# Kernel optimization log

Measured on AMD Instinct MI355X. Metric: run time of the kernel, lower is better.

## Reference

```python
import jax, jax.numpy as jnp
import numpy as np

M, L, P, KK = 8, 3, 12, 9  # n_heads, n_levels, n_points, patch_size**2

def lrelu(v):
    return jnp.where(v >= 0, v, 0.1 * v)

def conv2d(x, w, b, pad):
    y = jax.lax.conv_general_dilated(x, w, (1, 1), [(pad, pad), (pad, pad)], dimension_numbers=('NCHW', 'OIHW', 'NCHW'))
    return y + b[None, :, None, None]

def trunk(x, w1, b1, w2, b2, w3, b3, w4, b4):
    h = lrelu(conv2d(x, w1, b1, 0))
    h = lrelu(conv2d(h, w2, b2, 1))
    h = lrelu(conv2d(h, w3, b3, 1))
    return conv2d(h, w4, b4, 0)

def grid_sample(img, gx, gy, align_corners):
    # img [N,C,H,W]; gx,gy [N,Q] normalized to [-1,1]; bilinear, zeros padding
    N, C, H, W = img.shape
    if align_corners:
        ix = (gx + 1.0) * 0.5 * (W - 1)
        iy = (gy + 1.0) * 0.5 * (H - 1)
    else:
        ix = ((gx + 1.0) * W - 1.0) * 0.5
        iy = ((gy + 1.0) * H - 1.0) * 0.5
    ix0 = jnp.floor(ix); iy0 = jnp.floor(iy)
    wx1 = ix - ix0; wy1 = iy - iy0
    flat = img.reshape(N, C, H * W)
    def gather(xi, yi, wgt):
        valid = (xi >= 0) & (xi <= W - 1) & (yi >= 0) & (yi <= H - 1)
        idx = (jnp.clip(yi, 0, H - 1) * W + jnp.clip(xi, 0, W - 1)).astype(jnp.int32)
        v = jnp.take_along_axis(flat, idx[:, None, :], axis=2)
        return v * (wgt * valid)[:, None, :]
    return (gather(ix0, iy0, (1 - wx1) * (1 - wy1)) + gather(ix0 + 1, iy0, wx1 * (1 - wy1))
            + gather(ix0, iy0 + 1, (1 - wx1) * wy1) + gather(ix0 + 1, iy0 + 1, wx1 * wy1))

def flow_warp(img, flow):
    # img [n,c,h,w]; flow [n,2,h,w] in pixels; torch grid_sample align_corners=True, zeros padding
    n, c, h, w = img.shape
    gy, gx = jnp.meshgrid(jnp.arange(h, dtype=img.dtype), jnp.arange(w, dtype=img.dtype), indexing='ij')
    gxn = 2.0 * (gx[None] + flow[:, 0]) / max(w - 1, 1) - 1.0
    gyn = 2.0 * (gy[None] + flow[:, 1]) / max(h - 1, 1) - 1.0
    return grid_sample(img, gxn.reshape(n, -1), gyn.reshape(n, -1), True).reshape(n, c, h, w)

def msdeform_attn(value, loc, attn, h, w):
    # pytorch MSDeformAttn core: value [N,L*HW,M,D]; loc [N,HW,M,L,Pt,2]; attn [N,HW,M,L,Pt]
    N, _, _, D = value.shape
    HW = h * w
    Pt = loc.shape[4]
    grids = 2.0 * loc - 1.0
    sampled = []
    for l in range(L):
        v = value[:, l * HW:(l + 1) * HW].transpose(0, 2, 3, 1).reshape(N * M, D, h, w)
        g = grids[:, :, :, l].transpose(0, 2, 1, 3, 4).reshape(N * M, HW * Pt, 2)
        s = grid_sample(v, g[..., 0], g[..., 1], False)  # [N*M, D, HW*Pt]
        sampled.append(s.reshape(N * M, D, HW, Pt))
    sampled = jnp.concatenate(sampled, axis=-1)  # [N*M, D, HW, L*Pt]
    aw = attn.transpose(0, 2, 1, 3, 4).reshape(N * M, HW, L * Pt)
    out = jnp.einsum('ndqp,nqp->nqd', sampled, aw)
    return out.reshape(N, M, HW, D).transpose(0, 2, 1, 3).reshape(N, HW, M * D)

def _forward(x, flow_1, flow_2, flip_flow_1, flip_flow_2, aw_w1, aw_b1, aw_w2, aw_b2, aw_w3, aw_b3, aw_w4, aw_b4, so_w1, so_b1, so_w2, so_b2, so_w3, so_b3, so_w4, so_b4, po_w1, po_b1, po_w2, po_b2, po_w3, po_b3, po_w4, po_b4, vp_w, vp_b, op_w1, op_b1, op_w2, op_b2):
    n, t, c, h, w = x.shape
    HW = h * w
    flow_cn1 = flow_1
    flow_cn2 = flow_1 + flow_warp(flow_2, flow_cn1)
    warp1 = flow_warp(x[:, 1], flow_cn1)
    warp2 = flow_warp(x[:, 2], flow_cn2)
    extra = jnp.concatenate([x[:, 0], warp1, warp2, flow_cn1, flow_cn2], axis=1)  # [n, 3c+4, h, w]
    value = conv2d(x.reshape(n, t * c, h, w), vp_w, vp_b, 0)
    off = trunk(extra, so_w1, so_b1, so_w2, so_b2, so_w3, so_b3, so_w4, so_b4)
    aw = trunk(extra, aw_w1, aw_b1, aw_w2, aw_b2, aw_w3, aw_b3, aw_w4, aw_b4)
    po = trunk(extra, po_w1, po_b1, po_w2, po_b2, po_w3, po_b3, po_w4, po_b4)
    value = value.reshape(n, t, c, HW).transpose(0, 1, 3, 2).reshape(n, t * HW, M, c // M)
    off = off.reshape(n, -1, HW).transpose(0, 2, 1).reshape(n, HW, M, L, P, 2)
    po = po.reshape(n, -1, HW).transpose(0, 2, 1).reshape(n, HW, M, L, P)
    po = jax.nn.sigmoid(po) * 3.0
    aw = aw.reshape(n, -1, HW).transpose(0, 2, 1).reshape(n, HW, M, L * P * KK)
    aw = jax.nn.softmax(aw, axis=-1).reshape(n, HW, M, L, P * KK)
    # flow-guided per-level offsets: level0 zeros, level1 flow_cn1, level2 flow_cn2
    f1 = flow_cn1.reshape(n, 2, HW).transpose(0, 2, 1)
    f2 = flow_cn2.reshape(n, 2, HW).transpose(0, 2, 1)
    fstack = jnp.stack([jnp.zeros_like(f1), f1, f2], axis=2)  # [n,HW,L,2]
    off = off + fstack[:, :, None, :, None, :]
    # 3x3 patch around each sampling point, scaled by learned patch offsets
    a = jnp.arange(-1, 2, dtype=x.dtype)
    pnx, pny = jnp.meshgrid(a, a, indexing='ij')
    p_n = jnp.stack([pnx, pny], axis=-1).reshape(KK, 2)
    off = off[..., None, :] + p_n * po[..., None, None]  # [n,HW,M,L,P,KK,2]
    off = off.reshape(n, HW, M, L, P * KK, 2)
    # reference points (valid ratios == 1)
    ry = (jnp.arange(h, dtype=x.dtype) + 0.5) / h
    rx = (jnp.arange(w, dtype=x.dtype) + 0.5) / w
    gy, gx = jnp.meshgrid(ry, rx, indexing='ij')
    ref = jnp.stack([gx, gy], axis=-1).reshape(1, HW, 1, 1, 1, 2)
    norm = jnp.array([w, h], dtype=x.dtype)
    loc = ref + off / norm
    out = msdeform_attn(value, loc, aw, h, w)  # [n, HW, c]
    feat = out.reshape(n, h, w, c).transpose(0, 3, 1, 2)
    res = conv2d(lrelu(conv2d(feat, op_w1, op_b1, 0)), op_w2, op_b2, 0)
    return res + x[:, 0]

def setup_inputs():
    key = jax.random.key(0)
    keys = jax.random.split(key, 64)
    it = iter(range(64))
    def nrm(shape, scale):
        return jax.random.normal(keys[next(it)], shape, jnp.float32) * scale
    n, t, c, h, w = 1, 3, 64, 64, 64
    Cin = t * c + 4  # 196
    d = {}
    d['x'] = nrm((n, t, c, h, w), 1.0)
    for nm in ['flow_1', 'flow_2', 'flip_flow_1', 'flip_flow_2']:
        d[nm] = nrm((n, 2, h, w), 1.5)
    def branch(prefix, out_ch, final_scale):
        d[prefix + '_w1'] = nrm((64, Cin, 1, 1), 1.0 / np.sqrt(Cin))
        d[prefix + '_b1'] = nrm((64,), 0.01)
        d[prefix + '_w2'] = nrm((64, 64, 3, 3), 1.0 / np.sqrt(64 * 9))
        d[prefix + '_b2'] = nrm((64,), 0.01)
        d[prefix + '_w3'] = nrm((64, 64, 3, 3), 1.0 / np.sqrt(64 * 9))
        d[prefix + '_b3'] = nrm((64,), 0.01)
        d[prefix + '_w4'] = nrm((out_ch, 64, 1, 1), final_scale)
        d[prefix + '_b4'] = nrm((out_ch,), 0.01)
    branch('aw', M * L * P * KK, 0.01)
    branch('so', M * L * P * 2, 0.01)
    branch('po', M * L * P, 0.01)
    d['vp_w'] = nrm((t * c, t * c, 1, 1), 1.0 / np.sqrt(t * c))
    d['vp_b'] = nrm((t * c,), 0.01)
    d['op_w1'] = nrm((c, c, 1, 1), 1.0 / np.sqrt(c))
    d['op_b1'] = nrm((c,), 0.01)
    d['op_w2'] = nrm((c, c, 1, 1), 1.0 / np.sqrt(c))
    d['op_b2'] = nrm((c,), 0.01)
    return d

def reference(x, flow_1, flow_2, flip_flow_1, flip_flow_2, aw_w1, aw_b1, aw_w2, aw_b2, aw_w3, aw_b3, aw_w4, aw_b4, so_w1, so_b1, so_w2, so_b2, so_w3, so_b3, so_w4, so_b4, po_w1, po_b1, po_w2, po_b2, po_w3, po_b3, po_w4, po_b4, vp_w, vp_b, op_w1, op_b1, op_w2, op_b2):
    return _forward(x, flow_1, flow_2, flip_flow_1, flip_flow_2, aw_w1, aw_b1, aw_w2, aw_b2, aw_w3, aw_b3, aw_w4, aw_b4, so_w1, so_b1, so_w2, so_b2, so_w3, so_b3, so_w4, so_b4, po_w1, po_b1, po_w2, po_b2, po_w3, po_b3, po_w4, po_b4, vp_w, vp_b, op_w1, op_b1, op_w2, op_b2)
```

## Files before the change

kernel.cpp:

```cpp
#include <hip/hip_runtime.h>
#include <hip/hip_bf16.h>
#include <math.h>

#define HWN 4096
#define VROW 72
#define VYP 36
#define VSZ_SH (24 * VYP * VROW * 16)

typedef __attribute__((ext_vector_type(8))) short short8;
typedef __attribute__((ext_vector_type(4))) float f32x4;

__device__ __forceinline__ float lrelu_f(float v) { return v >= 0.f ? v : 0.1f * v; }

__device__ __forceinline__ unsigned short f2bf(float f) {
  union { float f; unsigned u; } v; v.f = f;
  unsigned r = v.u + 0x7fff + ((v.u >> 16) & 1);
  return (unsigned short)(r >> 16);
}
__device__ __forceinline__ float bf2f(unsigned short u) {
  union { unsigned u; float f; } v; v.u = ((unsigned)u) << 16;
  return v.f;
}
__device__ __forceinline__ float bf_lo(unsigned u) {
  union { unsigned u; float f; } v; v.u = u << 16; return v.f;
}
__device__ __forceinline__ float bf_hi(unsigned u) {
  union { unsigned u; float f; } v; v.u = u & 0xffff0000u; return v.f;
}

__device__ __forceinline__ float bilin_zero(const float* __restrict__ img, float ix, float iy) {
  float fx0 = floorf(ix), fy0 = floorf(iy);
  int x0 = (int)fx0, y0 = (int)fy0;
  float wx1 = ix - fx0, wy1 = iy - fy0;
  float wx0 = 1.f - wx1, wy0 = 1.f - wy1;
  float acc = 0.f;
  if ((unsigned)y0 < 64u) {
    if ((unsigned)x0 < 64u)       acc += wx0 * wy0 * img[y0 * 64 + x0];
    if ((unsigned)(x0 + 1) < 64u) acc += wx1 * wy0 * img[y0 * 64 + x0 + 1];
  }
  if ((unsigned)(y0 + 1) < 64u) {
    if ((unsigned)x0 < 64u)       acc += wx0 * wy1 * img[(y0 + 1) * 64 + x0];
    if ((unsigned)(x0 + 1) < 64u) acc += wx1 * wy1 * img[(y0 + 1) * 64 + x0 + 1];
  }
  return acc;
}

__global__ void k_pre(
    const float* __restrict__ x, const float* __restrict__ flow1, const float* __restrict__ flow2,
    const float* so_w4, const float* po_w4, const float* aw_w4,
    const float* so_b4, const float* po_b4, const float* aw_b4,
    const float* so_b1, const float* po_b1, const float* aw_b1,
    const float* so_b2, const float* po_b2, const float* aw_b2,
    const float* so_b3, const float* po_b3, const float* aw_b3,
    const float* so_w1, const float* po_w1, const float* aw_w1,
    const float* so_w2, const float* po_w2, const float* aw_w2,
    const float* so_w3, const float* po_w3, const float* aw_w3,
    const float* op_w1, const float* op_w2, const float* vp_w,
    unsigned short* Wtail, float* btail, float* b1c, float* b2c, float* b3c,
    unsigned short* o1b, unsigned short* o2b, unsigned short* W1,
    unsigned short* W2g, unsigned short* W3g, unsigned short* vpb,
    unsigned short* xb, float* fcn2, unsigned short* vA) {
  __shared__ unsigned short tile[64 * 65];
  __shared__ unsigned short wrow[576];
  int gx = blockIdx.x;
  int tid = threadIdx.x;
  if (gx < 864) {
    int t = gx * 256 + tid;
    int row = t >> 6, k = t & 63;
    float v = row < 576 ? so_w4[row * 64 + k]
            : row < 864 ? po_w4[(row - 576) * 64 + k]
                        : aw_w4[(row - 864) * 64 + k];
    Wtail[t] = f2bf(v);
  } else if (gx < 912) {
    int t = (gx - 864) * 256 + tid;
    if (t < 3456) {
      btail[t] = t < 576 ? so_b4[t] : t < 864 ? po_b4[t - 576] : aw_b4[t - 864];
    } else if (t < 3648) {
      int i = t - 3456; b1c[i] = i < 64 ? so_b1[i] : i < 128 ? po_b1[i - 64] : aw_b1[i - 128];
    } else if (t < 3840) {
      int i = t - 3648; b2c[i] = i < 64 ? so_b2[i] : i < 128 ? po_b2[i - 64] : aw_b2[i - 128];
    } else if (t < 4032) {
      int i = t - 3840; b3c[i] = i < 64 ? so_b3[i] : i < 128 ? po_b3[i - 64] : aw_b3[i - 128];
    } else if (t < 8128) {
      o1b[t - 4032] = f2bf(op_w1[t - 4032]);
    } else if (t < 12224) {
      o2b[t - 8128] = f2bf(op_w2[t - 8128]);
    }
  } else if (gx < 1080) {
    int t = (gx - 912) * 256 + tid;
    if (t < 192 * 224) {
      int row = t / 224, k = t % 224;
      int tr = row >> 6, lco = row & 63;
      const float* s = tr == 0 ? so_w1 : tr == 1 ? po_w1 : aw_w1;
      W1[t] = (k < 196) ? f2bf(s[lco * 196 + k]) : (unsigned short)0;
    }
  } else if (gx < 1464) {
    int b = gx - 1080;
    int which = b >= 192;
    b &= 191;
    int tr = b >> 6, co = b & 63;
    const float* s;
    if (!which) s = tr == 0 ? so_w2 : tr == 1 ? po_w2 : aw_w2;
    else        s = tr == 0 ? so_w3 : tr == 1 ? po_w3 : aw_w3;
    unsigned short* d = which ? W3g : W2g;
#pragma unroll
    for (int j = tid; j < 576; j += 256) wrow[j] = f2bf(s[co * 576 + j]);
    __syncthreads();
#pragma unroll
    for (int j = tid; j < 576; j += 256)
      d[((size_t)tr * 64 + co) * 576 + j] = wrow[(j & 63) * 9 + (j >> 6)];
  } else if (gx < 1608) {
    int t = (gx - 1464) * 256 + tid;
    if (t < 192 * 192) vpb[t] = f2bf(vp_w[t]);
  } else if (gx < 1800) {
    int b = gx - 1608;
    int ptile = b & 63, cg = b >> 6;
    int px = tid & 63, ch0 = (tid >> 6) * 16;
#pragma unroll
    for (int i = 0; i < 16; i++) {
      float v = x[(size_t)(cg * 64 + ch0 + i) * HWN + ptile * 64 + px];
      tile[(ch0 + i) * 65 + px] = f2bf(v);
    }
    __syncthreads();
    int c = tid & 63, pl0 = (tid >> 6) * 16;
#pragma unroll
    for (int i = 0; i < 16; i++)
      xb[(size_t)(ptile * 64 + pl0 + i) * 192 + cg * 64 + c] = tile[c * 65 + pl0 + i];
  } else if (gx < 1816) {
    int p = (gx - 1800) * 256 + tid;
    int px = p & 63, py = p >> 6;
    float fx = flow1[p], fy = flow1[HWN + p];
    float ix = (float)px + fx, iy = (float)py + fy;
    fcn2[p] = fx + bilin_zero(flow2, ix, iy);
    fcn2[HWN + p] = fy + bilin_zero(flow2 + HWN, ix, iy);
  } else {
    int i = (gx - 1816) * 256 + tid;
    if (i < 2 * VSZ_SH / 8) ((uint4*)vA)[i] = make_uint4(0, 0, 0, 0);
  }
}

__global__ void k_extra(const unsigned short* __restrict__ xb, const float* __restrict__ flow1,
                        const float* __restrict__ fcn2, unsigned short* __restrict__ extra) {
  int w = threadIdx.x >> 6, c = threadIdx.x & 63;
  int p = blockIdx.x * 4 + w;
  int px = p & 63, py = p >> 6;
  float fx1 = flow1[p], fy1 = flow1[HWN + p];
  float fx2 = fcn2[p],  fy2 = fcn2[HWN + p];
  extra[(size_t)p * 224 + c] = xb[(size_t)p * 192 + c];
#pragma unroll
  for (int lev = 0; lev < 2; lev++) {
    float ix = (float)px + (lev ? fx2 : fx1);
    float iy = (float)py + (lev ? fy2 : fy1);
    float fx0 = floorf(ix), fy0 = floorf(iy);
    int x0 = (int)fx0, y0 = (int)fy0;
    float wx1 = ix - fx0, wy1 = iy - fy0;
    float wx0 = 1.f - wx1, wy0 = 1.f - wy1;
    int coff = (lev + 1) * 64;
    float acc = 0.f;
    if ((unsigned)y0 < 64u) {
      if ((unsigned)x0 < 64u)       acc += wx0 * wy0 * bf2f(xb[(size_t)(y0 * 64 + x0) * 192 + coff + c]);
      if ((unsigned)(x0 + 1) < 64u) acc += wx1 * wy0 * bf2f(xb[(size_t)(y0 * 64 + x0 + 1) * 192 + coff + c]);
    }
    if ((unsigned)(y0 + 1) < 64u) {
      if ((unsigned)x0 < 64u)       acc += wx0 * wy1 * bf2f(xb[(size_t)((y0 + 1) * 64 + x0) * 192 + coff + c]);
      if ((unsigned)(x0 + 1) < 64u) acc += wx1 * wy1 * bf2f(xb[(size_t)((y0 + 1) * 64 + x0 + 1) * 192 + coff + c]);
    }
    extra[(size_t)p * 224 + coff + c] = f2bf(acc);
  }
  if (c < 2) {
    extra[(size_t)p * 224 + 192 + c] = f2bf(flow1[c * HWN + p]);
    extra[(size_t)p * 224 + 194 + c] = f2bf(fcn2[c * HWN + p]);
  }
  if (c < 28) extra[(size_t)p * 224 + 196 + c] = 0;
}

__global__ __launch_bounds__(128) void k_gemm2(
    const unsigned short* __restrict__ A0, const unsigned short* __restrict__ Wm0,
    const float* __restrict__ bias0, unsigned short* __restrict__ out0,
    const unsigned short* __restrict__ A1, const unsigned short* __restrict__ Wm1,
    const float* __restrict__ bias1, unsigned short* __restrict__ out1) {
  int z = blockIdx.z;
  const unsigned short* A = z ? A1 : A0;
  const unsigned short* Wm = z ? Wm1 : Wm0;
  const float* bias = z ? bias1 : bias0;
  unsigned short* out = z ? out1 : out0;
  int K = z ? 224 : 192;

  int wv = threadIdx.x >> 6;
  int l = threadIdx.x & 63;
  int lm = l & 15, lq = l >> 4;
  int p0 = blockIdx.x * 32 + wv * 16;
  int co0 = blockIdx.y * 32;

  f32x4 acc[2];
#pragma unroll
  for (int nt = 0; nt < 2; nt++) {
    float bv = bias[co0 + nt * 16 + lm];
    acc[nt] = (f32x4){bv, bv, bv, bv};
  }
  const unsigned short* ap = A + (size_t)(p0 + lm) * K + lq * 8;
  const unsigned short* wp = Wm + (size_t)(co0 + lm) * K + lq * 8;
  for (int k0 = 0; k0 < K; k0 += 32) {
    short8 af = *(const short8*)(ap + k0);
#pragma unroll
    for (int nt = 0; nt < 2; nt++) {
      short8 bf = *(const short8*)(wp + (size_t)nt * 16 * K + k0);
      acc[nt] = __builtin_amdgcn_mfma_f32_16x16x32_bf16(af, bf, acc[nt], 0, 0, 0);
    }
  }
#pragma unroll
  for (int nt = 0; nt < 2; nt++) {
    int co = co0 + nt * 16 + lm;
#pragma unroll
    for (int r = 0; r < 4; r++) {
      int p = p0 + lq * 4 + r;
      float v = acc[nt][r];
      if (z) v = lrelu_f(v);
      out[(size_t)p * 192 + co] = f2bf(v);
    }
  }
}

__global__ __launch_bounds__(128) void k_conv3g(const unsigned short* __restrict__ h,
                                                const unsigned short* __restrict__ Wm,
                                                const float* __restrict__ bias,
                                                unsigned short* __restrict__ out) {
  int wv = threadIdx.x >> 6;
  int l = threadIdx.x & 63;
  int lm = l & 15, lq = l >> 4;
  int p0 = blockIdx.x * 32 + wv * 16;
  int co0 = blockIdx.y * 16;
  int t = blockIdx.z;
  int p = p0 + lm;
  int px = p & 63, py = p >> 6;

  float bv = bias[t * 64 + co0 + lm];
  f32x4 acc = (f32x4){bv, bv, bv, bv};
  const unsigned short* wp = Wm + ((size_t)t * 64 + co0 + lm) * 576 + lq * 8;
#pragma unroll
  for (int kidx = 0; kidx < 9; kidx++) {
    int ky = kidx / 3, kx = kidx % 3;
    int pp = p + (ky - 1) * 64 + (kx - 1);
    bool valid = ((unsigned)(px + kx - 1) < 64u) && ((unsigned)(py + ky - 1) < 64u);
    const unsigned short* apb = h + (size_t)pp * 192 + t * 64 + lq * 8;
#pragma unroll
    for (int c2 = 0; c2 < 2; c2++) {
      short8 af = {};
      if (valid) af = *(const short8*)(apb + c2 * 32);
      short8 bf = *(const short8*)(wp + kidx * 64 + c2 * 32);
      acc = __builtin_amdgcn_mfma_f32_16x16x32_bf16(af, bf, acc, 0, 0, 0);
    }
  }
#pragma unroll
  for (int r = 0; r < 4; r++) {
    int po_ = p0 + lq * 4 + r;
    out[(size_t)po_ * 192 + t * 64 + co0 + lm] = f2bf(lrelu_f(acc[r]));
  }
}

__global__ __launch_bounds__(256) void k_tail(const unsigned short* __restrict__ A,
                                              const unsigned short* __restrict__ Wm,
                                              const float* __restrict__ bias,
                                              unsigned short* __restrict__ out,
                                              const unsigned short* __restrict__ vsb,
                                              unsigned short* __restrict__ vA,
                                              unsigned short* __restrict__ vB) {
  if (blockIdx.y >= 108) {
    int i = ((blockIdx.y - 108) * 64 + blockIdx.x) * 256 + threadIdx.x;
    int lm = i % 24, p = i / 24;
    uint4 v = ((const uint4*)vsb)[p * 24 + lm];
    int y = p >> 6, xx = p & 63;
    int ypA = (y >> 1) + 1, slotA = y & 1;
    int ypB = (y + 1) >> 1, slotB = (y & 1) ^ 1;
    ((uint4*)vA)[((lm * VYP + ypA) * VROW + xx + 2) * 2 + slotA] = v;
    ((uint4*)vB)[((lm * VYP + ypB) * VROW + xx + 2) * 2 + slotB] = v;
    return;
  }
  int wv = threadIdx.x >> 6;
  int l = threadIdx.x & 63;
  int lm = l & 15, lq = l >> 4;
  int p0 = blockIdx.x * 64 + wv * 16;
  int co0 = blockIdx.y * 32;
  int t = (co0 < 576) ? 0 : (co0 < 864 ? 1 : 2);

  f32x4 acc[2];
#pragma unroll
  for (int nt = 0; nt < 2; nt++) {
    float bv = bias[co0 + nt * 16 + lm];
    acc[nt] = (f32x4){bv, bv, bv, bv};
  }
  const unsigned short* ap = A + (size_t)(p0 + lm) * 192 + t * 64 + lq * 8;
  const unsigned short* wp = Wm + (size_t)(co0 + lm) * 64 + lq * 8;
#pragma unroll
  for (int k0 = 0; k0 < 64; k0 += 32) {
    short8 af = *(const short8*)(ap + k0);
#pragma unroll
    for (int nt = 0; nt < 2; nt++) {
      short8 bf = *(const short8*)(wp + (size_t)nt * 16 * 64 + k0);
      acc[nt] = __builtin_amdgcn_mfma_f32_16x16x32_bf16(af, bf, acc[nt], 0, 0, 0);
    }
  }
#pragma unroll
  for (int nt = 0; nt < 2; nt++) {
    int co = co0 + nt * 16 + lm;
#pragma unroll
    for (int r = 0; r < 4; r++) {
      int p = p0 + lq * 4 + r;
      float v = acc[nt][r];
      if (t == 2) v = __expf(v);
      else if (t == 1) v = 3.f * __builtin_amdgcn_rcpf(1.f + __expf(-v));
      out[(size_t)p * 3456 + co] = f2bf(v);
    }
  }
}

__global__ __launch_bounds__(256, 4) void k_msdeform(
    const unsigned short* __restrict__ vA,
    const unsigned short* __restrict__ to,
    const float* __restrict__ flow1, const float* __restrict__ fcn2,
    unsigned short* __restrict__ featb) {
  int yl = threadIdx.x & 15;
  int p = blockIdx.x * 16 + (threadIdx.x >> 4);
  int m = blockIdx.y;
  int px = p & 63, py = p >> 6;

  float fx1 = flow1[p], fy1 = flow1[HWN + p];
  float fx2 = fcn2[p],  fy2 = fcn2[HWN + p];

  const unsigned short* row = to + (size_t)p * 3456;

  float acc[8];
#pragma unroll
  for (int d = 0; d < 8; d++) acc[d] = 0.f;
  float wsum = 0.f;

#pragma unroll 1
  for (int pair = yl; pair < 36; pair += 16) {
    int lv = pair / 12, pt = pair % 12;
    float fx = (lv == 1) ? fx1 : ((lv == 2) ? fx2 : 0.f);
    float fy = (lv == 1) ? fy1 : ((lv == 2) ? fy2 : 0.f);
    int ch = (m * 3 + lv) * 12 + pt;
    unsigned ow = *(const unsigned*)(row + ch * 2);
    float ox = bf_lo(ow);
    float oy = bf_hi(ow);
    float s = bf2f(row[576 + ch]);
    float bx = (float)px + ox + fx;
    float by = (float)py + oy + fy;
    int lmoff = (lv * 8 + m) * (VYP * VROW * 16);
    const unsigned short* lgp = row + 864 + m * 324 + lv * 108 + pt * 9;
#pragma unroll 3
    for (int kk = 0; kk < 9; kk++) {
      float pnx = (float)(kk / 3 - 1);
      float pny = (float)(kk % 3 - 1);
      float ix = bx + pnx * s;
      float iy = by + pny * s;
      float wgt = bf2f(lgp[kk]);
      wsum += wgt;

      float fx0 = floorf(ix), fy0 = floorf(iy);
      float wx1 = ix - fx0, wy1 = iy - fy0;
      float wx0 = 1.f - wx1, wy0 = 1.f - wy1;
      int x0 = min(max((int)fx0, -2), 66);
      int y0 = min(max((int)fy0, -2), 66);
      int par = y0 & 1;
      int yp = (y0 + 2 - par) >> 1;
      const unsigned short* vb = vA + par * VSZ_SH;
      int idx = lmoff + (yp * VROW + x0 + 2) * 16;

      uint4 q0 = *(const uint4*)(vb + idx);
      uint4 q1 = *(const uint4*)(vb + idx + 8);
      uint4 q2 = *(const uint4*)(vb + idx + 16);
      uint4 q3 = *(const uint4*)(vb + idx + 24);

      float w00 = wgt * wx0 * wy0, w01 = wgt * wx0 * wy1;
      float w10 = wgt * wx1 * wy0, w11 = wgt * wx1 * wy1;

      acc[0] += w00 * bf_lo(q0.x) + w01 * bf_lo(q1.x) + w10 * bf_lo(q2.x) + w11 * bf_lo(q3.x);
      acc[1] += w00 * bf_hi(q0.x) + w01 * bf_hi(q1.x) + w10 * bf_hi(q2.x) + w11 * bf_hi(q3.x);
      acc[2] += w00 * bf_lo(q0.y) + w01 * bf_lo(q1.y) + w10 * bf_lo(q2.y) + w11 * bf_lo(q3.y);
      acc[3] += w00 * bf_hi(q0.y) + w01 * bf_hi(q1.y) + w10 * bf_hi(q2.y) + w11 * bf_hi(q3.y);
      acc[4] += w00 * bf_lo(q0.z) + w01 * bf_lo(q1.z) + w10 * bf_lo(q2.z) + w11 * bf_lo(q3.z);
      acc[5] += w00 * bf_hi(q0.z) + w01 * bf_hi(q1.z) + w10 * bf_hi(q2.z) + w11 * bf_hi(q3.z);
      acc[6] += w00 * bf_lo(q0.w) + w01 * bf_lo(q1.w) + w10 * bf_lo(q2.w) + w11 * bf_lo(q3.w);
      acc[7] += w00 * bf_hi(q0.w) + w01 * bf_hi(q1.w) + w10 * bf_hi(q2.w) + w11 * bf_hi(q3.w);
    }
  }
#pragma unroll
  for (int mask = 1; mask < 16; mask <<= 1) {
    wsum += __shfl_xor(wsum, mask);
#pragma unroll
    for (int d = 0; d < 8; d++) acc[d] += __shfl_xor(acc[d], mask);
  }
  if (yl < 8) {
    float inv = __builtin_amdgcn_rcpf(wsum);
    float r = 0.f;
#pragma unroll
    for (int d = 0; d < 8; d++) r = (d == yl) ? acc[d] : r;
    featb[(size_t)p * 64 + m * 8 + yl] = f2bf(r * inv);
  }
}

__global__ __launch_bounds__(256) void k_opout(const unsigned short* __restrict__ featb,
                                               const unsigned short* __restrict__ o1b,
                                               const float* __restrict__ bias1,
                                               const unsigned short* __restrict__ o2b,
                                               const float* __restrict__ bias2,
                                               const float* __restrict__ x,
                                               float* __restrict__ out) {
  __shared__ unsigned short hop[64 * 72];
  int wv = threadIdx.x >> 6;
  int l = threadIdx.x & 63;
  int lm = l & 15, lq = l >> 4;
  int bp0 = blockIdx.x * 64;

  f32x4 acc1[4];
#pragma unroll
  for (int nt = 0; nt < 4; nt++) {
    float bv = bias1[nt * 16 + lm];
    acc1[nt] = (f32x4){bv, bv, bv, bv};
  }
  const unsigned short* ap = featb + (size_t)(bp0 + wv * 16 + lm) * 64 + lq * 8;
#pragma unroll
  for (int k0 = 0; k0 < 64; k0 += 32) {
    short8 af = *(const short8*)(ap + k0);
#pragma unroll
    for (int nt = 0; nt < 4; nt++) {
      short8 bf = *(const short8*)(o1b + (size_t)(nt * 16 + lm) * 64 + lq * 8 + k0);
      acc1[nt] = __builtin_amdgcn_mfma_f32_16x16x32_bf16(af, bf, acc1[nt], 0, 0, 0);
    }
  }
#pragma unroll
  for (int nt = 0; nt < 4; nt++)
#pragma unroll
    for (int r = 0; r < 4; r++)
      hop[(wv * 16 + lq * 4 + r) * 72 + nt * 16 + lm] = f2bf(lrelu_f(acc1[nt][r]));
  __syncthreads();

  f32x4 b4;
#pragma unroll
  for (int r = 0; r < 4; r++) b4[r] = bias2[wv * 16 + lq * 4 + r];
  f32x4 acc2[4];
#pragma unroll
  for (int pg = 0; pg < 4; pg++) acc2[pg] = b4;
#pragma unroll
  for (int k0 = 0; k0 < 64; k0 += 32) {
    short8 af = *(const short8*)(o2b + (size_t)(wv * 16 + lm) * 64 + k0 + lq * 8);
#pragma unroll
    for (int pg = 0; pg < 4; pg++) {
      short8 bf = *(const short8*)(hop + (pg * 16 + lm) * 72 + k0 + lq * 8);
      acc2[pg] = __builtin_amdgcn_mfma_f32_16x16x32_bf16(af, bf, acc2[pg], 0, 0, 0);
    }
  }
#pragma unroll
  for (int pg = 0; pg < 4; pg++) {
#pragma unroll
    for (int r = 0; r < 4; r++) {
      int co = wv * 16 + lq * 4 + r;
      int p = bp0 + pg * 16 + lm;
      out[(size_t)co * HWN + p] = acc2[pg][r] + x[(size_t)co * HWN + p];
    }
  }
}

extern "C" void kernel_launch(void* const* d_in, const int* in_sizes, int n_in,
                              void* d_out, int out_size, void* d_ws, size_t ws_size,
                              hipStream_t stream) {
  const float* x     = (const float*)d_in[0];
  const float* flow1 = (const float*)d_in[1];
  const float* flow2 = (const float*)d_in[2];
  const float* aw_w1 = (const float*)d_in[5];
  const float* aw_b1 = (const float*)d_in[6];
  const float* aw_w2 = (const float*)d_in[7];
  const float* aw_b2 = (const float*)d_in[8];
  const float* aw_w3 = (const float*)d_in[9];
  const float* aw_b3 = (const float*)d_in[10];
  const float* aw_w4 = (const float*)d_in[11];
  const float* aw_b4 = (const float*)d_in[12];
  const float* so_w1 = (const float*)d_in[13];
  const float* so_b1 = (const float*)d_in[14];
  const float* so_w2 = (const float*)d_in[15];
  const float* so_b2 = (const float*)d_in[16];
  const float* so_w3 = (const float*)d_in[17];
  const float* so_b3 = (const float*)d_in[18];
  const float* so_w4 = (const float*)d_in[19];
  const float* so_b4 = (const float*)d_in[20];
  const float* po_w1 = (const float*)d_in[21];
  const float* po_b1 = (const float*)d_in[22];
  const float* po_w2 = (const float*)d_in[23];
  const float* po_b2 = (const float*)d_in[24];
  const float* po_w3 = (const float*)d_in[25];
  const float* po_b3 = (const float*)d_in[26];
  const float* po_w4 = (const float*)d_in[27];
  const float* po_b4 = (const float*)d_in[28];
  const float* vp_w  = (const float*)d_in[29];
  const float* vp_b  = (const float*)d_in[30];
  const float* op_w1 = (const float*)d_in[31];
  const float* op_b1 = (const float*)d_in[32];
  const float* op_w2 = (const float*)d_in[33];
  const float* op_b2 = (const float*)d_in[34];

  char* base = (char*)d_ws;
  size_t off = 0;
  auto alloc = [&](size_t bytes) { void* pp = base + off; off = (off + bytes + 255) & ~(size_t)255; return pp; };

  float* fcn2  = (float*)alloc(2 * HWN * 4);
  unsigned short* xb    = (unsigned short*)alloc(192 * HWN * 2);
  unsigned short* vsb   = (unsigned short*)alloc(192 * HWN * 2);
  unsigned short* extra = (unsigned short*)alloc(224 * HWN * 2);
  unsigned short* h1    = (unsigned short*)alloc(192 * HWN * 2);
  unsigned short* h2    = (unsigned short*)alloc(192 * HWN * 2);
  unsigned short* h3    = (unsigned short*)alloc(192 * HWN * 2);
  unsigned short* to    = (unsigned short*)alloc((size_t)3456 * HWN * 2);
  unsigned short* featb = (unsigned short*)alloc(64 * HWN * 2);
  unsigned short* vA    = (unsigned short*)alloc((size_t)VSZ_SH * 2 * 2);
  unsigned short* vB    = vA + VSZ_SH;
  unsigned short* Wtail = (unsigned short*)alloc(3456 * 64 * 2);
  float* btail = (float*)alloc(3456 * 4);
  float* b1c   = (float*)alloc(192 * 4);
  float* b2c   = (float*)alloc(192 * 4);
  float* b3c   = (float*)alloc(192 * 4);
  unsigned short* o1b = (unsigned short*)alloc(64 * 64 * 2);
  unsigned short* o2b = (unsigned short*)alloc(64 * 64 * 2);
  unsigned short* W1  = (unsigned short*)alloc(192 * 224 * 2);
  unsigned short* W2g = (unsigned short*)alloc(3 * 64 * 576 * 2);
  unsigned short* W3g = (unsigned short*)alloc(3 * 64 * 576 * 2);
  unsigned short* vpb = (unsigned short*)alloc(192 * 192 * 2);

  k_pre<<<2788, 256, 0, stream>>>(
      x, flow1, flow2,
      so_w4, po_w4, aw_w4, so_b4, po_b4, aw_b4,
      so_b1, po_b1, aw_b1, so_b2, po_b2, aw_b2, so_b3, po_b3, aw_b3,
      so_w1, po_w1, aw_w1, so_w2, po_w2, aw_w2, so_w3, po_w3, aw_w3,
      op_w1, op_w2, vp_w,
      Wtail, btail, b1c, b2c, b3c, o1b, o2b, W1, W2g, W3g, vpb, xb, fcn2, vA);

  k_extra<<<1024, 256, 0, stream>>>(xb, flow1, fcn2, extra);

  k_gemm2<<<dim3(128, 6, 2), 128, 0, stream>>>(xb, vpb, vp_b, vsb, extra, W1, b1c, h1);

  k_conv3g<<<dim3(128, 4, 3), 128, 0, stream>>>(h1, W2g, b2c, h2);
  k_conv3g<<<dim3(128, 4, 3), 128, 0, stream>>>(h2, W3g, b3c, h3);
  k_tail<<<dim3(64, 114), 256, 0, stream>>>(h3, Wtail, btail, to, vsb, vA, vB);

  k_msdeform<<<dim3(256, 8), 256, 0, stream>>>(vA, to, flow1, fcn2, featb);

  k_opout<<<64, 256, 0, stream>>>(featb, o1b, op_b1, o2b, op_b2, x, (float*)d_out);
}
```

Measured before the change: 235.4 us.

## Merge all stages into one cooperative persistent kernel with grid syncs and fp8 values

Replaces the eight separate kernel launches with a single cooperative persistent kernel that walks over each former stage's block range and uses grid-wide barriers between stages. This is meant to remove launch gaps and tail effects between kernels. The value buffer appears to move to an fp8 layout unpacked with the packed fp8-to-f32 conversion, which halves gather traffic in deformable sampling at the cost of precision. The grid size is capped by occupancy, so stages with many small blocks run serially per CU, and each grid sync adds its own cost.

```diff
diff --git a/kernel.cpp b/kernel.cpp
--- a/kernel.cpp
+++ b/kernel.cpp
@@ -1,14 +1,16 @@
 #include <hip/hip_runtime.h>
 #include <hip/hip_bf16.h>
+#include <hip/hip_cooperative_groups.h>
 #include <math.h>
 
 #define HWN 4096
 #define VROW 72
 #define VYP 36
-#define VSZ_SH (24 * VYP * VROW * 16)
+#define VSZ_B (24 * VYP * VROW * 16)
 
 typedef __attribute__((ext_vector_type(8))) short short8;
 typedef __attribute__((ext_vector_type(4))) float f32x4;
+typedef __attribute__((ext_vector_type(2))) float f32x2;
 
 __device__ __forceinline__ float lrelu_f(float v) { return v >= 0.f ? v : 0.1f * v; }
 
@@ -18,14 +20,17 @@
   return (unsigned short)(r >> 16);
 }
 __device__ __forceinline__ float bf2f(unsigned short u) {
-  union { unsigned u; float f; } v; v.u = ((unsigned)u) << 16;
-  return v.f;
+  union { unsigned u; float f; } v; v.u = ((unsigned)u) << 16; return v.f;
 }
 __device__ __forceinline__ float bf_lo(unsigned u) {
   union { unsigned u; float f; } v; v.u = u << 16; return v.f;
 }
 __device__ __forceinline__ float bf_hi(unsigned u) {
   union { unsigned u; float f; } v; v.u = u & 0xffff0000u; return v.f;
+}
+template <bool HI>
+__device__ __forceinline__ f32x2 cvt8(unsigned u) {
+  return __builtin_amdgcn_cvt_pk_f32_fp8((int)u, HI);
 }
 
 __device__ __forceinline__ float bilin_zero(const float* __restrict__ img, float ix, float iy) {
@@ -45,192 +50,31 @@
   return acc;
 }
 
-__global__ void k_pre(
-    const float* __restrict__ x, const float* __restrict__ flow1, const float* __restrict__ flow2,
-    const float* so_w4, const float* po_w4, const float* aw_w4,
-    const float* so_b4, const float* po_b4, const float* aw_b4,
-    const float* so_b1, const float* po_b1, const float* aw_b1,
-    const float* so_b2, const float* po_b2, const float* aw_b2,
-    const float* so_b3, const float* po_b3, const float* aw_b3,
-    const float* so_w1, const float* po_w1, const float* aw_w1,
-    const float* so_w2, const float* po_w2, const float* aw_w2,
-    const float* so_w3, const float* po_w3, const float* aw_w3,
-    const float* op_w1, const float* op_w2, const float* vp_w,
-    unsigned short* Wtail, float* btail, float* b1c, float* b2c, float* b3c,
-    unsigned short* o1b, unsigned short* o2b, unsigned short* W1,
-    unsigned short* W2g, unsigned short* W3g, unsigned short* vpb,
-    unsigned short* xb, float* fcn2, unsigned short* vA) {
-  __shared__ unsigned short tile[64 * 65];
-  __shared__ unsigned short wrow[576];
-  int gx = blockIdx.x;
-  int tid = threadIdx.x;
-  if (gx < 864) {
-    int t = gx * 256 + tid;
-    int row = t >> 6, k = t & 63;
-    float v = row < 576 ? so_w4[row * 64 + k]
-            : row < 864 ? po_w4[(row - 576) * 64 + k]
-                        : aw_w4[(row - 864) * 64 + k];
-    Wtail[t] = f2bf(v);
-  } else if (gx < 912) {
-    int t = (gx - 864) * 256 + tid;
-    if (t < 3456) {
-      btail[t] = t < 576 ? so_b4[t] : t < 864 ? po_b4[t - 576] : aw_b4[t - 864];
-    } else if (t < 3648) {
-      int i = t - 3456; b1c[i] = i < 64 ? so_b1[i] : i < 128 ? po_b1[i - 64] : aw_b1[i - 128];
-    } else if (t < 3840) {
-      int i = t - 3648; b2c[i] = i < 64 ? so_b2[i] : i < 128 ? po_b2[i - 64] : aw_b2[i - 128];
-    } else if (t < 4032) {
-      int i = t - 3840; b3c[i] = i < 64 ? so_b3[i] : i < 128 ? po_b3[i - 64] : aw_b3[i - 128];
-    } else if (t < 8128) {
-      o1b[t - 4032] = f2bf(op_w1[t - 4032]);
-    } else if (t < 12224) {
-      o2b[t - 8128] = f2bf(op_w2[t - 8128]);
-    }
-  } else if (gx < 1080) {
-    int t = (gx - 912) * 256 + tid;
-    if (t < 192 * 224) {
-      int row = t / 224, k = t % 224;
-      int tr = row >> 6, lco = row & 63;
-      const float* s = tr == 0 ? so_w1 : tr == 1 ? po_w1 : aw_w1;
-      W1[t] = (k < 196) ? f2bf(s[lco * 196 + k]) : (unsigned short)0;
-    }
-  } else if (gx < 1464) {
-    int b = gx - 1080;
-    int which = b >= 192;
-    b &= 191;
-    int tr = b >> 6, co = b & 63;
-    const float* s;
-    if (!which) s = tr == 0 ? so_w2 : tr == 1 ? po_w2 : aw_w2;
-    else        s = tr == 0 ? so_w3 : tr == 1 ? po_w3 : aw_w3;
-    unsigned short* d = which ? W3g : W2g;
-#pragma unroll
-    for (int j = tid; j < 576; j += 256) wrow[j] = f2bf(s[co * 576 + j]);
-    __syncthreads();
-#pragma unroll
-    for (int j = tid; j < 576; j += 256)
-      d[((size_t)tr * 64 + co) * 576 + j] = wrow[(j & 63) * 9 + (j >> 6)];
-  } else if (gx < 1608) {
-    int t = (gx - 1464) * 256 + tid;
-    if (t < 192 * 192) vpb[t] = f2bf(vp_w[t]);
-  } else if (gx < 1800) {
-    int b = gx - 1608;
-    int ptile = b & 63, cg = b >> 6;
-    int px = tid & 63, ch0 = (tid >> 6) * 16;
-#pragma unroll
-    for (int i = 0; i < 16; i++) {
-      float v = x[(size_t)(cg * 64 + ch0 + i) * HWN + ptile * 64 + px];
-      tile[(ch0 + i) * 65 + px] = f2bf(v);
-    }
-    __syncthreads();
-    int c = tid & 63, pl0 = (tid >> 6) * 16;
-#pragma unroll
-    for (int i = 0; i < 16; i++)
-      xb[(size_t)(ptile * 64 + pl0 + i) * 192 + cg * 64 + c] = tile[c * 65 + pl0 + i];
-  } else if (gx < 1816) {
-    int p = (gx - 1800) * 256 + tid;
-    int px = p & 63, py = p >> 6;
-    float fx = flow1[p], fy = flow1[HWN + p];
-    float ix = (float)px + fx, iy = (float)py + fy;
-    fcn2[p] = fx + bilin_zero(flow2, ix, iy);
-    fcn2[HWN + p] = fy + bilin_zero(flow2 + HWN, ix, iy);
-  } else {
-    int i = (gx - 1816) * 256 + tid;
-    if (i < 2 * VSZ_SH / 8) ((uint4*)vA)[i] = make_uint4(0, 0, 0, 0);
-  }
-}
-
-__global__ void k_extra(const unsigned short* __restrict__ xb, const float* __restrict__ flow1,
-                        const float* __restrict__ fcn2, unsigned short* __restrict__ extra) {
-  int w = threadIdx.x >> 6, c = threadIdx.x & 63;
-  int p = blockIdx.x * 4 + w;
-  int px = p & 63, py = p >> 6;
-  float fx1 = flow1[p], fy1 = flow1[HWN + p];
-  float fx2 = fcn2[p],  fy2 = fcn2[HWN + p];
-  extra[(size_t)p * 224 + c] = xb[(size_t)p * 192 + c];
-#pragma unroll
-  for (int lev = 0; lev < 2; lev++) {
-    float ix = (float)px + (lev ? fx2 : fx1);
-    float iy = (float)py + (lev ? fy2 : fy1);
-    float fx0 = floorf(ix), fy0 = floorf(iy);
-    int x0 = (int)fx0, y0 = (int)fy0;
-    float wx1 = ix - fx0, wy1 = iy - fy0;
-    float wx0 = 1.f - wx1, wy0 = 1.f - wy1;
-    int coff = (lev + 1) * 64;
-    float acc = 0.f;
-    if ((unsigned)y0 < 64u) {
-      if ((unsigned)x0 < 64u)       acc += wx0 * wy0 * bf2f(xb[(size_t)(y0 * 64 + x0) * 192 + coff + c]);
-      if ((unsigned)(x0 + 1) < 64u) acc += wx1 * wy0 * bf2f(xb[(size_t)(y0 * 64 + x0 + 1) * 192 + coff + c]);
-    }
-    if ((unsigned)(y0 + 1) < 64u) {
-      if ((unsigned)x0 < 64u)       acc += wx0 * wy1 * bf2f(xb[(size_t)((y0 + 1) * 64 + x0) * 192 + coff + c]);
-      if ((unsigned)(x0 + 1) < 64u) acc += wx1 * wy1 * bf2f(xb[(size_t)((y0 + 1) * 64 + x0 + 1) * 192 + coff + c]);
-    }
-    extra[(size_t)p * 224 + coff + c] = f2bf(acc);
-  }
-  if (c < 2) {
-    extra[(size_t)p * 224 + 192 + c] = f2bf(flow1[c * HWN + p]);
-    extra[(size_t)p * 224 + 194 + c] = f2bf(fcn2[c * HWN + p]);
-  }
-  if (c < 28) extra[(size_t)p * 224 + 196 + c] = 0;
-}
-
-__global__ __launch_bounds__(128) void k_gemm2(
-    const unsigned short* __restrict__ A0, const unsigned short* __restrict__ Wm0,
-    const float* __restrict__ bias0, unsigned short* __restrict__ out0,
-    const unsigned short* __restrict__ A1, const unsigned short* __restrict__ Wm1,
-    const float* __restrict__ bias1, unsigned short* __restrict__ out1) {
-  int z = blockIdx.z;
-  const unsigned short* A = z ? A1 : A0;
-  const unsigned short* Wm = z ? Wm1 : Wm0;
-  const float* bias = z ? bias1 : bias0;
-  unsigned short* out = z ? out1 : out0;
-  int K = z ? 224 : 192;
-
-  int wv = threadIdx.x >> 6;
-  int l = threadIdx.x & 63;
+struct KP {
+  const float *x, *flow1, *flow2;
+  const float *so_w4, *po_w4, *aw_w4, *so_b4, *po_b4, *aw_b4;
+  const float *so_b1, *po_b1, *aw_b1, *so_b2, *po_b2, *aw_b2, *so_b3, *po_b3, *aw_b3;
+  const float *so_w1, *po_w1, *aw_w1, *so_w2, *po_w2, *aw_w2, *so_w3, *po_w3, *aw_w3;
+  const float *op_w1, *op_w2, *vp_w, *vp_b, *op_b1, *op_b2;
+  unsigned short *Wtail;
+  float *btail, *b1c, *b2c, *b3c;
+  unsigned short *o1b, *o2b, *W1, *W2g, *W3g, *vpb;
+  unsigned short *xb, *vsb, *extra, *h1, *h2, *h3, *to, *featb;
+  float *fcn2;
+  unsigned char *v8;
+  float *out;
+};
+
+__device__ __forceinline__ void conv3g_body(const KP& P, const unsigned short* __restrict__ h,
+                                            const unsigned short* __restrict__ Wm,
+                                            const float* __restrict__ bias,
+                                            unsigned short* __restrict__ out, int hb, int tid) {
+  int wv = tid >> 6;
+  int l = tid & 63;
   int lm = l & 15, lq = l >> 4;
-  int p0 = blockIdx.x * 32 + wv * 16;
-  int co0 = blockIdx.y * 32;
-
-  f32x4 acc[2];
-#pragma unroll
-  for (int nt = 0; nt < 2; nt++) {
-    float bv = bias[co0 + nt * 16 + lm];
-    acc[nt] = (f32x4){bv, bv, bv, bv};
-  }
-  const unsigned short* ap = A + (size_t)(p0 + lm) * K + lq * 8;
-  const unsigned short* wp = Wm + (size_t)(co0 + lm) * K + lq * 8;
-  for (int k0 = 0; k0 < K; k0 += 32) {
-    short8 af = *(const short8*)(ap + k0);
-#pragma unroll
-    for (int nt = 0; nt < 2; nt++) {
-      short8 bf = *(const short8*)(wp + (size_t)nt * 16 * K + k0);
-      acc[nt] = __builtin_amdgcn_mfma_f32_16x16x32_bf16(af, bf, acc[nt], 0, 0, 0);
-    }
-  }
-#pragma unroll
-  for (int nt = 0; nt < 2; nt++) {
-    int co = co0 + nt * 16 + lm;
-#pragma unroll
-    for (int r = 0; r < 4; r++) {
-      int p = p0 + lq * 4 + r;
-      float v = acc[nt][r];
-      if (z) v = lrelu_f(v);
-      out[(size_t)p * 192 + co] = f2bf(v);
-    }
-  }
-}
-
-__global__ __launch_bounds__(128) void k_conv3g(const unsigned short* __restrict__ h,
-                                                const unsigned short* __restrict__ Wm,
-                                                const float* __restrict__ bias,
-                                                unsigned short* __restrict__ out) {
-  int wv = threadIdx.x >> 6;
-  int l = threadIdx.x & 63;
-  int lm = l & 15, lq = l >> 4;
-  int p0 = blockIdx.x * 32 + wv * 16;
-  int co0 = blockIdx.y * 16;
-  int t = blockIdx.z;
+  int bx = hb & 127, by = (hb >> 7) & 3, t = hb >> 9;
+  int p0 = bx * 32 + wv * 16;
+  int co0 = by * 16;
   int p = p0 + lm;
   int px = p & 63, py = p >> 6;
 
@@ -258,206 +102,376 @@
   }
 }
 
-__global__ __launch_bounds__(256) void k_tail(const unsigned short* __restrict__ A,
-                                              const unsigned short* __restrict__ Wm,
-                                              const float* __restrict__ bias,
-                                              unsigned short* __restrict__ out,
-                                              const unsigned short* __restrict__ vsb,
-                                              unsigned short* __restrict__ vA,
-                                              unsigned short* __restrict__ vB) {
-  if (blockIdx.y >= 108) {
-    int i = ((blockIdx.y - 108) * 64 + blockIdx.x) * 256 + threadIdx.x;
-    int lm = i % 24, p = i / 24;
-    uint4 v = ((const uint4*)vsb)[p * 24 + lm];
-    int y = p >> 6, xx = p & 63;
-    int ypA = (y >> 1) + 1, slotA = y & 1;
-    int ypB = (y + 1) >> 1, slotB = (y & 1) ^ 1;
-    ((uint4*)vA)[((lm * VYP + ypA) * VROW + xx + 2) * 2 + slotA] = v;
-    ((uint4*)vB)[((lm * VYP + ypB) * VROW + xx + 2) * 2 + slotB] = v;
-    return;
-  }
-  int wv = threadIdx.x >> 6;
-  int l = threadIdx.x & 63;
-  int lm = l & 15, lq = l >> 4;
-  int p0 = blockIdx.x * 64 + wv * 16;
-  int co0 = blockIdx.y * 32;
-  int t = (co0 < 576) ? 0 : (co0 < 864 ? 1 : 2);
-
-  f32x4 acc[2];
-#pragma unroll
-  for (int nt = 0; nt < 2; nt++) {
-    float bv = bias[co0 + nt * 16 + lm];
-    acc[nt] = (f32x4){bv, bv, bv, bv};
-  }
-  const unsigned short* ap = A + (size_t)(p0 + lm) * 192 + t * 64 + lq * 8;
-  const unsigned short* wp = Wm + (size_t)(co0 + lm) * 64 + lq * 8;
-#pragma unroll
-  for (int k0 = 0; k0 < 64; k0 += 32) {
-    short8 af = *(const short8*)(ap + k0);
-#pragma unroll
-    for (int nt = 0; nt < 2; nt++) {
-      short8 bf = *(const short8*)(wp + (size_t)nt * 16 * 64 + k0);
-      acc[nt] = __builtin_amdgcn_mfma_f32_16x16x32_bf16(af, bf, acc[nt], 0, 0, 0);
-    }
-  }
-#pragma unroll
-  for (int nt = 0; nt < 2; nt++) {
-    int co = co0 + nt * 16 + lm;
-#pragma unroll
-    for (int r = 0; r < 4; r++) {
-      int p = p0 + lq * 4 + r;
-      float v = acc[nt][r];
-      if (t == 2) v = __expf(v);
-      else if (t == 1) v = 3.f * __builtin_amdgcn_rcpf(1.f + __expf(-v));
-      out[(size_t)p * 3456 + co] = f2bf(v);
-    }
-  }
-}
-
-__global__ __launch_bounds__(256, 4) void k_msdeform(
-    const unsigned short* __restrict__ vA,
-    const unsigned short* __restrict__ to,
-    const float* __restrict__ flow1, const float* __restrict__ fcn2,
-    unsigned short* __restrict__ featb) {
-  int yl = threadIdx.x & 15;
-  int p = blockIdx.x * 16 + (threadIdx.x >> 4);
-  int m = blockIdx.y;
-  int px = p & 63, py = p >> 6;
-
-  float fx1 = flow1[p], fy1 = flow1[HWN + p];
-  float fx2 = fcn2[p],  fy2 = fcn2[HWN + p];
-
-  const unsigned short* row = to + (size_t)p * 3456;
-
-  float acc[8];
-#pragma unroll
-  for (int d = 0; d < 8; d++) acc[d] = 0.f;
-  float wsum = 0.f;
-
-#pragma unroll 1
-  for (int pair = yl; pair < 36; pair += 16) {
-    int lv = pair / 12, pt = pair % 12;
-    float fx = (lv == 1) ? fx1 : ((lv == 2) ? fx2 : 0.f);
-    float fy = (lv == 1) ? fy1 : ((lv == 2) ? fy2 : 0.f);
-    int ch = (m * 3 + lv) * 12 + pt;
-    unsigned ow = *(const unsigned*)(row + ch * 2);
-    float ox = bf_lo(ow);
-    float oy = bf_hi(ow);
-    float s = bf2f(row[576 + ch]);
-    float bx = (float)px + ox + fx;
-    float by = (float)py + oy + fy;
-    int lmoff = (lv * 8 + m) * (VYP * VROW * 16);
-    const unsigned short* lgp = row + 864 + m * 324 + lv * 108 + pt * 9;
-#pragma unroll 3
-    for (int kk = 0; kk < 9; kk++) {
-      float pnx = (float)(kk / 3 - 1);
-      float pny = (float)(kk % 3 - 1);
-      float ix = bx + pnx * s;
-      float iy = by + pny * s;
-      float wgt = bf2f(lgp[kk]);
-      wsum += wgt;
-
+__global__ __launch_bounds__(256, 4) void k_all(KP P) {
+  namespace cg = cooperative_groups;
+  cg::grid_group grid = cg::this_grid();
+  __shared__ __align__(16) unsigned short smem[4608];
+  int tid = threadIdx.x;
+  int NB = gridDim.x;
+
+  for (int gx = blockIdx.x; gx < 2302; gx += NB) {
+    __syncthreads();
+    if (gx < 864) {
+      int t = gx * 256 + tid;
+      int row = t >> 6, k = t & 63;
+      float v = row < 576 ? P.so_w4[row * 64 + k]
+              : row < 864 ? P.po_w4[(row - 576) * 64 + k]
+                          : P.aw_w4[(row - 864) * 64 + k];
+      P.Wtail[t] = f2bf(v);
+    } else if (gx < 912) {
+      int t = (gx - 864) * 256 + tid;
+      if (t < 3456) {
+        P.btail[t] = t < 576 ? P.so_b4[t] : t < 864 ? P.po_b4[t - 576] : P.aw_b4[t - 864];
+      } else if (t < 3648) {
+        int i = t - 3456; P.b1c[i] = i < 64 ? P.so_b1[i] : i < 128 ? P.po_b1[i - 64] : P.aw_b1[i - 128];
+      } else if (t < 3840) {
+        int i = t - 3648; P.b2c[i] = i < 64 ? P.so_b2[i] : i < 128 ? P.po_b2[i - 64] : P.aw_b2[i - 128];
+      } else if (t < 4032) {
+        int i = t - 3840; P.b3c[i] = i < 64 ? P.so_b3[i] : i < 128 ? P.po_b3[i - 64] : P.aw_b3[i - 128];
+      } else if (t < 8128) {
+        P.o1b[t - 4032] = f2bf(P.op_w1[t - 4032]);
+      } else if (t < 12224) {
+        P.o2b[t - 8128] = f2bf(P.op_w2[t - 8128]);
+      }
+    } else if (gx < 1080) {
+      int t = (gx - 912) * 256 + tid;
+      if (t < 192 * 224) {
+        int row = t / 224, k = t % 224;
+        int tr = row >> 6, lco = row & 63;
+        const float* s = tr == 0 ? P.so_w1 : tr == 1 ? P.po_w1 : P.aw_w1;
+        P.W1[t] = (k < 196) ? f2bf(s[lco * 196 + k]) : (unsigned short)0;
+      }
+    } else if (gx < 1464) {
+      int b = gx - 1080;
+      int which = b >= 192;
+      b &= 191;
+      int tr = b >> 6, co = b & 63;
+      const float* s;
+      if (!which) s = tr == 0 ? P.so_w2 : tr == 1 ? P.po_w2 : P.aw_w2;
+      else        s = tr == 0 ? P.so_w3 : tr == 1 ? P.po_w3 : P.aw_w3;
+      unsigned short* d = which ? P.W3g : P.W2g;
+      for (int j = tid; j < 576; j += 256) smem[j] = f2bf(s[co * 576 + j]);
+      __syncthreads();
+      for (int j = tid; j < 576; j += 256)
+        d[((size_t)tr * 64 + co) * 576 + j] = smem[(j & 63) * 9 + (j >> 6)];
+    } else if (gx < 1608) {
+      int t = (gx - 1464) * 256 + tid;
+      if (t < 192 * 192) P.vpb[t] = f2bf(P.vp_w[t]);
+    } else if (gx < 1800) {
+      int b = gx - 1608;
+      int ptile = b & 63, cg2 = b >> 6;
+      int px = tid & 63, ch0 = (tid >> 6) * 16;
+#pragma unroll
+      for (int i = 0; i < 16; i++) {
+        float v = P.x[(size_t)(cg2 * 64 + ch0 + i) * HWN + ptile * 64 + px];
+        smem[(ch0 + i) * 65 + px] = f2bf(v);
+      }
+      __syncthreads();
+      int c = tid & 63, pl0 = (tid >> 6) * 16;
+#pragma unroll
+      for (int i = 0; i < 16; i++)
+        P.xb[(size_t)(ptile * 64 + pl0 + i) * 192 + cg2 * 64 + c] = smem[c * 65 + pl0 + i];
+    } else if (gx < 1816) {
+      int p = (gx - 1800) * 256 + tid;
+      int px = p & 63, py = p >> 6;
+      float fx = P.flow1[p], fy = P.flow1[HWN + p];
+      float ix = (float)px + fx, iy = (float)py + fy;
+      P.fcn2[p] = fx + bilin_zero(P.flow2, ix, iy);
+      P.fcn2[HWN + p] = fy + bilin_zero(P.flow2 + HWN, ix, iy);
+    } else {
+      int i = (gx - 1816) * 256 + tid;
+      if (i < 2 * VSZ_B / 16) ((uint4*)P.v8)[i] = make_uint4(0, 0, 0, 0);
+    }
+  }
+  grid.sync();
+
+  for (int vb = blockIdx.x; vb < 1024; vb += NB) {
+    int w = tid >> 6, c = tid & 63;
+    int p = vb * 4 + w;
+    int px = p & 63, py = p >> 6;
+    float fx1 = P.flow1[p], fy1 = P.flow1[HWN + p];
+    float fx2 = P.fcn2[p],  fy2 = P.fcn2[HWN + p];
+    P.extra[(size_t)p * 224 + c] = P.xb[(size_t)p * 192 + c];
+#pragma unroll
+    for (int lev = 0; lev < 2; lev++) {
+      float ix = (float)px + (lev ? fx2 : fx1);
+      float iy = (float)py + (lev ? fy2 : fy1);
       float fx0 = floorf(ix), fy0 = floorf(iy);
+      int x0 = (int)fx0, y0 = (int)fy0;
       float wx1 = ix - fx0, wy1 = iy - fy0;
       float wx0 = 1.f - wx1, wy0 = 1.f - wy1;
-      int x0 = min(max((int)fx0, -2), 66);
-      int y0 = min(max((int)fy0, -2), 66);
-      int par = y0 & 1;
-      int yp = (y0 + 2 - par) >> 1;
-      const unsigned short* vb = vA + par * VSZ_SH;
-      int idx = lmoff + (yp * VROW + x0 + 2) * 16;
-
-      uint4 q0 = *(const uint4*)(vb + idx);
-      uint4 q1 = *(const uint4*)(vb + idx + 8);
-      uint4 q2 = *(const uint4*)(vb + idx + 16);
-      uint4 q3 = *(const uint4*)(vb + idx + 24);
-
-      float w00 = wgt * wx0 * wy0, w01 = wgt * wx0 * wy1;
-      float w10 = wgt * wx1 * wy0, w11 = wgt * wx1 * wy1;
-
-      acc[0] += w00 * bf_lo(q0.x) + w01 * bf_lo(q1.x) + w10 * bf_lo(q2.x) + w11 * bf_lo(q3.x);
-      acc[1] += w00 * bf_hi(q0.x) + w01 * bf_hi(q1.x) + w10 * bf_hi(q2.x) + w11 * bf_hi(q3.x);
-      acc[2] += w00 * bf_lo(q0.y) + w01 * bf_lo(q1.y) + w10 * bf_lo(q2.y) + w11 * bf_lo(q3.y);
-      acc[3] += w00 * bf_hi(q0.y) + w01 * bf_hi(q1.y) + w10 * bf_hi(q2.y) + w11 * bf_hi(q3.y);
-      acc[4] += w00 * bf_lo(q0.z) + w01 * bf_lo(q1.z) + w10 * bf_lo(q2.z) + w11 * bf_lo(q3.z);
-      acc[5] += w00 * bf_hi(q0.z) + w01 * bf_hi(q1.z) + w10 * bf_hi(q2.z) + w11 * bf_hi(q3.z);
-      acc[6] += w00 * bf_lo(q0.w) + w01 * bf_lo(q1.w) + w10 * bf_lo(q2.w) + w11 * bf_lo(q3.w);
-      acc[7] += w00 * bf_hi(q0.w) + w01 * bf_hi(q1.w) + w10 * bf_hi(q2.w) + w11 * bf_hi(q3.w);
-    }
-  }
-#pragma unroll
-  for (int mask = 1; mask < 16; mask <<= 1) {
-    wsum += __shfl_xor(wsum, mask);
-#pragma unroll
-    for (int d = 0; d < 8; d++) acc[d] += __shfl_xor(acc[d], mask);
-  }
-  if (yl < 8) {
-    float inv = __builtin_amdgcn_rcpf(wsum);
-    float r = 0.f;
-#pragma unroll
-    for (int d = 0; d < 8; d++) r = (d == yl) ? acc[d] : r;
-    featb[(size_t)p * 64 + m * 8 + yl] = f2bf(r * inv);
-  }
-}
-
-__global__ __launch_bounds__(256) void k_opout(const unsigned short* __restrict__ featb,
-                                               const unsigned short* __restrict__ o1b,
-                                               const float* __restrict__ bias1,
-                                               const unsigned short* __restrict__ o2b,
-                                               const float* __restrict__ bias2,
-                                               const float* __restrict__ x,
-                                               float* __restrict__ out) {
-  __shared__ unsigned short hop[64 * 72];
-  int wv = threadIdx.x >> 6;
-  int l = threadIdx.x & 63;
-  int lm = l & 15, lq = l >> 4;
-  int bp0 = blockIdx.x * 64;
-
-  f32x4 acc1[4];
-#pragma unroll
-  for (int nt = 0; nt < 4; nt++) {
-    float bv = bias1[nt * 16 + lm];
-    acc1[nt] = (f32x4){bv, bv, bv, bv};
-  }
-  const unsigned short* ap = featb + (size_t)(bp0 + wv * 16 + lm) * 64 + lq * 8;
-#pragma unroll
-  for (int k0 = 0; k0 < 64; k0 += 32) {
-    short8 af = *(const short8*)(ap + k0);
+      int coff = (lev + 1) * 64;
+      float acc = 0.f;
+      if ((unsigned)y0 < 64u) {
+        if ((unsigned)x0 < 64u)       acc += wx0 * wy0 * bf2f(P.xb[(size_t)(y0 * 64 + x0) * 192 + coff + c]);
+        if ((unsigned)(x0 + 1) < 64u) acc += wx1 * wy0 * bf2f(P.xb[(size_t)(y0 * 64 + x0 + 1) * 192 + coff + c]);
+      }
+      if ((unsigned)(y0 + 1) < 64u) {
+        if ((unsigned)x0 < 64u)       acc += wx0 * wy1 * bf2f(P.xb[(size_t)((y0 + 1) * 64 + x0) * 192 + coff + c]);
+        if ((unsigned)(x0 + 1) < 64u) acc += wx1 * wy1 * bf2f(P.xb[(size_t)((y0 + 1) * 64 + x0 + 1) * 192 + coff + c]);
+      }
+      P.extra[(size_t)p * 224 + coff + c] = f2bf(acc);
+    }
+    if (c < 2) {
+      P.extra[(size_t)p * 224 + 192 + c] = f2bf(P.flow1[c * HWN + p]);
+      P.extra[(size_t)p * 224 + 194 + c] = f2bf(P.fcn2[c * HWN + p]);
+    }
+    if (c < 28) P.extra[(size_t)p * 224 + 196 + c] = 0;
+  }
+  grid.sync();
+
+  for (int vb = blockIdx.x; vb < 768; vb += NB) {
+    int t128 = tid & 127;
+    int hb = vb * 2 + (tid >> 7);
+    int z = hb >= 768;
+    int hbl = hb - z * 768;
+    int bx = hbl & 127, by = hbl >> 7;
+    const unsigned short* A = z ? P.extra : P.xb;
+    const unsigned short* Wm = z ? P.W1 : P.vpb;
+    const float* bias = z ? P.b1c : P.vp_b;
+    unsigned short* out = z ? P.h1 : P.vsb;
+    int K = z ? 224 : 192;
+
+    int wv = t128 >> 6;
+    int l = t128 & 63;
+    int lm = l & 15, lq = l >> 4;
+    int p0 = bx * 32 + wv * 16;
+    int co0 = by * 32;
+
+    f32x4 acc[2];
+#pragma unroll
+    for (int nt = 0; nt < 2; nt++) {
+      float bv = bias[co0 + nt * 16 + lm];
+      acc[nt] = (f32x4){bv, bv, bv, bv};
+    }
+    const unsigned short* ap = A + (size_t)(p0 + lm) * K + lq * 8;
+    const unsigned short* wp = Wm + (size_t)(co0 + lm) * K + lq * 8;
+    for (int k0 = 0; k0 < K; k0 += 32) {
+      short8 af = *(const short8*)(ap + k0);
+#pragma unroll
+      for (int nt = 0; nt < 2; nt++) {
+        short8 bf = *(const short8*)(wp + (size_t)nt * 16 * K + k0);
+        acc[nt] = __builtin_amdgcn_mfma_f32_16x16x32_bf16(af, bf, acc[nt], 0, 0, 0);
+      }
+    }
+#pragma unroll
+    for (int nt = 0; nt < 2; nt++) {
+      int co = co0 + nt * 16 + lm;
+#pragma unroll
+      for (int r = 0; r < 4; r++) {
+        int p = p0 + lq * 4 + r;
+        float v = acc[nt][r];
+        if (z) v = lrelu_f(v);
+        out[(size_t)p * 192 + co] = f2bf(v);
+      }
+    }
+  }
+  grid.sync();
+
+  for (int vb = blockIdx.x; vb < 768; vb += NB)
+    conv3g_body(P, P.h1, P.W2g, P.b2c, P.h2, vb * 2 + (tid >> 7), tid & 127);
+  grid.sync();
+  for (int vb = blockIdx.x; vb < 768; vb += NB)
+    conv3g_body(P, P.h2, P.W3g, P.b3c, P.h3, vb * 2 + (tid >> 7), tid & 127);
+  grid.sync();
+
+  for (int v = blockIdx.x; v < 7296; v += NB) {
+    int bx = v & 63, by = v >> 6;
+    if (by >= 108) {
+      int i = ((by - 108) * 64 + bx) * 256 + tid;
+      int lm = i % 24, p = i / 24;
+      uint4 vv = ((const uint4*)P.vsb)[p * 24 + lm];
+      int lo = 0, hi = 0;
+      lo = __builtin_amdgcn_cvt_pk_fp8_f32(bf_lo(vv.x), bf_hi(vv.x), lo, false);
+      lo = __builtin_amdgcn_cvt_pk_fp8_f32(bf_lo(vv.y), bf_hi(vv.y), lo, true);
+      hi = __builtin_amdgcn_cvt_pk_fp8_f32(bf_lo(vv.z), bf_hi(vv.z), hi, false);
+      hi = __builtin_amdgcn_cvt_pk_fp8_f32(bf_lo(vv.w), bf_hi(vv.w), hi, true);
+      uint2 pk; pk.x = (unsigned)lo; pk.y = (unsigned)hi;
+      int y = p >> 6, xx = p & 63;
+      int ypA = (y >> 1) + 1, slotA = y & 1;
+      int ypB = (y + 1) >> 1, slotB = (y & 1) ^ 1;
+      *(uint2*)(P.v8 + (((lm * VYP + ypA) * VROW + xx + 2) * 16 + slotA * 8)) = pk;
+      *(uint2*)(P.v8 + VSZ_B + (((lm * VYP + ypB) * VROW + xx + 2) * 16 + slotB * 8)) = pk;
+    } else {
+      int wv = tid >> 6;
+      int l = tid & 63;
+      int lm = l & 15, lq = l >> 4;
+      int p0 = bx * 64 + wv * 16;
+      int co0 = by * 32;
+      int t = (co0 < 576) ? 0 : (co0 < 864 ? 1 : 2);
+
+      f32x4 acc[2];
+#pragma unroll
+      for (int nt = 0; nt < 2; nt++) {
+        float bv = P.btail[co0 + nt * 16 + lm];
+        acc[nt] = (f32x4){bv, bv, bv, bv};
+      }
+      const unsigned short* ap = P.h3 + (size_t)(p0 + lm) * 192 + t * 64 + lq * 8;
+      const unsigned short* wp = P.Wtail + (size_t)(co0 + lm) * 64 + lq * 8;
+#pragma unroll
+      for (int k0 = 0; k0 < 64; k0 += 32) {
+        short8 af = *(const short8*)(ap + k0);
+#pragma unroll
+        for (int nt = 0; nt < 2; nt++) {
+          short8 bf = *(const short8*)(wp + (size_t)nt * 16 * 64 + k0);
+          acc[nt] = __builtin_amdgcn_mfma_f32_16x16x32_bf16(af, bf, acc[nt], 0, 0, 0);
+        }
+      }
+#pragma unroll
+      for (int nt = 0; nt < 2; nt++) {
+        int co = co0 + nt * 16 + lm;
+#pragma unroll
+        for (int r = 0; r < 4; r++) {
+          int p = p0 + lq * 4 + r;
+          float vv2 = acc[nt][r];
+          if (t == 2) vv2 = __expf(vv2);
+          else if (t == 1) vv2 = 3.f * __builtin_amdgcn_rcpf(1.f + __expf(-vv2));
+          P.to[(size_t)p * 3456 + co] = f2bf(vv2);
+        }
+      }
+    }
+  }
+  grid.sync();
+
+  for (int v = blockIdx.x; v < 2048; v += NB) {
+    int yl = tid & 15;
+    int p = (v & 255) * 16 + (tid >> 4);
+    int m = v >> 8;
+    int px = p & 63, py = p >> 6;
+
+    float fx1 = P.flow1[p], fy1 = P.flow1[HWN + p];
+    float fx2 = P.fcn2[p],  fy2 = P.fcn2[HWN + p];
+
+    const unsigned short* row = P.to + (size_t)p * 3456;
+
+    float acc[8];
+#pragma unroll
+    for (int d = 0; d < 8; d++) acc[d] = 0.f;
+    float wsum = 0.f;
+
+#pragma unroll 1
+    for (int pair = yl; pair < 36; pair += 16) {
+      int lv = pair / 12, pt = pair % 12;
+      float fx = (lv == 1) ? fx1 : ((lv == 2) ? fx2 : 0.f);
+      float fy = (lv == 1) ? fy1 : ((lv == 2) ? fy2 : 0.f);
+      int ch = (m * 3 + lv) * 12 + pt;
+      unsigned ow = *(const unsigned*)(row + ch * 2);
+      float ox = bf_lo(ow);
+      float oy = bf_hi(ow);
+      float s = bf2f(row[576 + ch]);
+      float bx = (float)px + ox + fx;
+      float by = (float)py + oy + fy;
+      int lmoff = (lv * 8 + m) * (VYP * VROW * 16);
+      const unsigned short* lgp = row + 864 + m * 324 + lv * 108 + pt * 9;
+#pragma unroll 3
+      for (int kk = 0; kk < 9; kk++) {
+        float pnx = (float)(kk / 3 - 1);
+        float pny = (float)(kk % 3 - 1);
+        float ix = bx + pnx * s;
+        float iy = by + pny * s;
+        float wgt = bf2f(lgp[kk]);
+        wsum += wgt;
+
+        float fx0 = floorf(ix), fy0 = floorf(iy);
+        float wx1 = ix - fx0, wy1 = iy - fy0;
+        float wx0 = 1.f - wx1, wy0 = 1.f - wy1;
+        int x0 = min(max((int)fx0, -2), 66);
+        int y0 = min(max((int)fy0, -2), 66);
+        int par = y0 & 1;
+        int yp = (y0 + 2 - par) >> 1;
+        const unsigned char* vb2 = P.v8 + par * VSZ_B + lmoff + (yp * VROW + x0 + 2) * 16;
+
+        uint4 qa = *(const uint4*)vb2;
+        uint4 qb = *(const uint4*)(vb2 + 16);
+
+        float w00 = wgt * wx0 * wy0, w01 = wgt * wx0 * wy1;
+        float w10 = wgt * wx1 * wy0, w11 = wgt * wx1 * wy1;
+
+        f32x2 a0 = cvt8<false>(qa.x), a1 = cvt8<true>(qa.x), a2 = cvt8<false>(qa.y), a3 = cvt8<true>(qa.y);
+        f32x2 b0 = cvt8<false>(qa.z), b1 = cvt8<true>(qa.z), b2 = cvt8<false>(qa.w), b3 = cvt8<true>(qa.w);
+        f32x2 c0 = cvt8<false>(qb.x), c1 = cvt8<true>(qb.x), c2 = cvt8<false>(qb.y), c3 = cvt8<true>(qb.y);
+        f32x2 d0 = cvt8<false>(qb.z), d1 = cvt8<true>(qb.z), d2 = cvt8<false>(qb.w), d3 = cvt8<true>(qb.w);
+
+        acc[0] += w00 * a0.x + w01 * b0.x + w10 * c0.x + w11 * d0.x;
+        acc[1] += w00 * a0.y + w01 * b0.y + w10 * c0.y + w11 * d0.y;
+        acc[2] += w00 * a1.x + w01 * b1.x + w10 * c1.x + w11 * d1.x;
+        acc[3] += w00 * a1.y + w01 * b1.y + w10 * c1.y + w11 * d1.y;
+        acc[4] += w00 * a2.x + w01 * b2.x + w10 * c2.x + w11 * d2.x;
+        acc[5] += w00 * a2.y + w01 * b2.y + w10 * c2.y + w11 * d2.y;
+        acc[6] += w00 * a3.x + w01 * b3.x + w10 * c3.x + w11 * d3.x;
+        acc[7] += w00 * a3.y + w01 * b3.y + w10 * c3.y + w11 * d3.y;
+      }
+    }
+#pragma unroll
+    for (int mask = 1; mask < 16; mask <<= 1) {
+      wsum += __shfl_xor(wsum, mask);
+#pragma unroll
+      for (int d = 0; d < 8; d++) acc[d] += __shfl_xor(acc[d], mask);
+    }
+    if (yl < 8) {
+      float inv = __builtin_amdgcn_rcpf(wsum);
+      float r = 0.f;
+#pragma unroll
+      for (int d = 0; d < 8; d++) r = (d == yl) ? acc[d] : r;
+      P.featb[(size_t)p * 64 + m * 8 + yl] = f2bf(r * inv);
+    }
+  }
+  grid.sync();
+
+  for (int vb = blockIdx.x; vb < 64; vb += NB) {
+    __syncthreads();
+    unsigned short* hop = smem;
+    int wv = tid >> 6;
+    int l = tid & 63;
+    int lm = l & 15, lq = l >> 4;
+    int bp0 = vb * 64;
+
+    f32x4 acc1[4];
 #pragma unroll
     for (int nt = 0; nt < 4; nt++) {
-      short8 bf = *(const short8*)(o1b + (size_t)(nt * 16 + lm) * 64 + lq * 8 + k0);
-      acc1[nt] = __builtin_amdgcn_mfma_f32_16x16x32_bf16(af, bf, acc1[nt], 0, 0, 0);
-    }
-  }
-#pragma unroll
-  for (int nt = 0; nt < 4; nt++)
-#pragma unroll
-    for (int r = 0; r < 4; r++)
-      hop[(wv * 16 + lq * 4 + r) * 72 + nt * 16 + lm] = f2bf(lrelu_f(acc1[nt][r]));
-  __syncthreads();
-
-  f32x4 b4;
-#pragma unroll
-  for (int r = 0; r < 4; r++) b4[r] = bias2[wv * 16 + lq * 4 + r];
-  f32x4 acc2[4];
-#pragma unroll
-  for (int pg = 0; pg < 4; pg++) acc2[pg] = b4;
-#pragma unroll
-  for (int k0 = 0; k0 < 64; k0 += 32) {
-    short8 af = *(const short8*)(o2b + (size_t)(wv * 16 + lm) * 64 + k0 + lq * 8);
+      float bv = P.op_b1[nt * 16 + lm];
+      acc1[nt] = (f32x4){bv, bv, bv, bv};
+    }
+    const unsigned short* ap = P.featb + (size_t)(bp0 + wv * 16 + lm) * 64 + lq * 8;
+#pragma unroll
+    for (int k0 = 0; k0 < 64; k0 += 32) {
+      short8 af = *(const short8*)(ap + k0);
+#pragma unroll
+      for (int nt = 0; nt < 4; nt++) {
+        short8 bf = *(const short8*)(P.o1b + (size_t)(nt * 16 + lm) * 64 + lq * 8 + k0);
+        acc1[nt] = __builtin_amdgcn_mfma_f32_16x16x32_bf16(af, bf, acc1[nt], 0, 0, 0);
+      }
+    }
+#pragma unroll
+    for (int nt = 0; nt < 4; nt++)
+#pragma unroll
+      for (int r = 0; r < 4; r++)
+        hop[(wv * 16 + lq * 4 + r) * 72 + nt * 16 + lm] = f2bf(lrelu_f(acc1[nt][r]));
+    __syncthreads();
+
+    f32x4 b4;
+#pragma unroll
+    for (int r = 0; r < 4; r++) b4[r] = P.op_b2[wv * 16 + lq * 4 + r];
+    f32x4 acc2[4];
+#pragma unroll
+    for (int pg = 0; pg < 4; pg++) acc2[pg] = b4;
+#pragma unroll
+    for (int k0 = 0; k0 < 64; k0 += 32) {
+      short8 af = *(const short8*)(P.o2b + (size_t)(wv * 16 + lm) * 64 + k0 + lq * 8);
+#pragma unroll
+      for (int pg = 0; pg < 4; pg++) {
+        short8 bf = *(const short8*)(hop + (pg * 16 + lm) * 72 + k0 + lq * 8);
+        acc2[pg] = __builtin_amdgcn_mfma_f32_16x16x32_bf16(af, bf, acc2[pg], 0, 0, 0);
+      }
+    }
 #pragma unroll
     for (int pg = 0; pg < 4; pg++) {
-      short8 bf = *(const short8*)(hop + (pg * 16 + lm) * 72 + k0 + lq * 8);
-      acc2[pg] = __builtin_amdgcn_mfma_f32_16x16x32_bf16(af, bf, acc2[pg], 0, 0, 0);
-    }
-  }
-#pragma unroll
-  for (int pg = 0; pg < 4; pg++) {
-#pragma unroll
-    for (int r = 0; r < 4; r++) {
-      int co = wv * 16 + lq * 4 + r;
-      int p = bp0 + pg * 16 + lm;
-      out[(size_t)co * HWN + p] = acc2[pg][r] + x[(size_t)co * HWN + p];
+#pragma unroll
+      for (int r = 0; r < 4; r++) {
+        int co = wv * 16 + lq * 4 + r;
+        int p = bp0 + pg * 16 + lm;
+        P.out[(size_t)co * HWN + p] = acc2[pg][r] + P.x[(size_t)co * HWN + p];
+      }
     }
   }
 }
@@ -465,84 +479,59 @@
 extern "C" void kernel_launch(void* const* d_in, const int* in_sizes, int n_in,
                               void* d_out, int out_size, void* d_ws, size_t ws_size,
                               hipStream_t stream) {
-  const float* x     = (const float*)d_in[0];
-  const float* flow1 = (const float*)d_in[1];
-  const float* flow2 = (const float*)d_in[2];
-  const float* aw_w1 = (const float*)d_in[5];
-  const float* aw_b1 = (const float*)d_in[6];
-  const float* aw_w2 = (const float*)d_in[7];
-  const float* aw_b2 = (const float*)d_in[8];
-  const float* aw_w3 = (const float*)d_in[9];
-  const float* aw_b3 = (const float*)d_in[10];
-  const float* aw_w4 = (const float*)d_in[11];
-  const float* aw_b4 = (const float*)d_in[12];
-  const float* so_w1 = (const float*)d_in[13];
-  const float* so_b1 = (const float*)d_in[14];
-  const float* so_w2 = (const float*)d_in[15];
-  const float* so_b2 = (const float*)d_in[16];
-  const float* so_w3 = (const float*)d_in[17];
-  const float* so_b3 = (const float*)d_in[18];
-  const float* so_w4 = (const float*)d_in[19];
-  const float* so_b4 = (const float*)d_in[20];
-  const float* po_w1 = (const float*)d_in[21];
-  const float* po_b1 = (const float*)d_in[22];
-  const float* po_w2 = (const float*)d_in[23];
-  const float* po_b2 = (const float*)d_in[24];
-  const float* po_w3 = (const float*)d_in[25];
-  const float* po_b3 = (const float*)d_in[26];
-  const float* po_w4 = (const float*)d_in[27];
-  const float* po_b4 = (const float*)d_in[28];
-  const float* vp_w  = (const float*)d_in[29];
-  const float* vp_b  = (const float*)d_in[30];
-  const float* op_w1 = (const float*)d_in[31];
-  const float* op_b1 = (const float*)d_in[32];
-  const float* op_w2 = (const float*)d_in[33];
-  const float* op_b2 = (const float*)d_in[34];
-
   char* base = (char*)d_ws;
   size_t off = 0;
   auto alloc = [&](size_t bytes) { void* pp = base + off; off = (off + bytes + 255) & ~(size_t)255; return pp; };
 
-  float* fcn2  = (float*)alloc(2 * HWN * 4);
-  unsigned short* xb    = (unsigned short*)alloc(192 * HWN * 2);
-  unsigned short* vsb   = (unsigned short*)alloc(192 * HWN * 2);
-  unsigned short* extra = (unsigned short*)alloc(224 * HWN * 2);
-  unsigned short* h1    = (unsigned short*)alloc(192 * HWN * 2);
-  unsigned short* h2    = (unsigned short*)alloc(192 * HWN * 2);
-  unsigned short* h3    = (unsigned short*)alloc(192 * HWN * 2);
-  unsigned short* to    = (unsigned short*)alloc((size_t)3456 * HWN * 2);
-  unsigned short* featb = (unsigned short*)alloc(64 * HWN * 2);
-  unsigned short* vA    = (unsigned short*)alloc((size_t)VSZ_SH * 2 * 2);
-  unsigned short* vB    = vA + VSZ_SH;
-  unsigned short* Wtail = (unsigned short*)alloc(3456 * 64 * 2);
-  float* btail = (float*)alloc(3456 * 4);
-  float* b1c   = (float*)alloc(192 * 4);
-  float* b2c   = (float*)alloc(192 * 4);
-  float* b3c   = (float*)alloc(192 * 4);
-  unsigned short* o1b = (unsigned short*)alloc(64 * 64 * 2);
-  unsigned short* o2b = (unsigned short*)alloc(64 * 64 * 2);
-  unsigned short* W1  = (unsigned short*)alloc(192 * 224 * 2);
-  unsigned short* W2g = (unsigned short*)alloc(3 * 64 * 576 * 2);
-  unsigned short* W3g = (unsigned short*)alloc(3 * 64 * 576 * 2);
-  unsigned short* vpb = (unsigned short*)alloc(192 * 192 * 2);
-
-  k_pre<<<2788, 256, 0, stream>>>(
-      x, flow1, flow2,
-      so_w4, po_w4, aw_w4, so_b4, po_b4, aw_b4,
-      so_b1, po_b1, aw_b1, so_b2, po_b2, aw_b2, so_b3, po_b3, aw_b3,
-      so_w1, po_w1, aw_w1, so_w2, po_w2, aw_w2, so_w3, po_w3, aw_w3,
-      op_w1, op_w2, vp_w,
-      Wtail, btail, b1c, b2c, b3c, o1b, o2b, W1, W2g, W3g, vpb, xb, fcn2, vA);
-
-  k_extra<<<1024, 256, 0, stream>>>(xb, flow1, fcn2, extra);
-
-  k_gemm2<<<dim3(128, 6, 2), 128, 0, stream>>>(xb, vpb, vp_b, vsb, extra, W1, b1c, h1);
-
-  k_conv3g<<<dim3(128, 4, 3), 128, 0, stream>>>(h1, W2g, b2c, h2);
-  k_conv3g<<<dim3(128, 4, 3), 128, 0, stream>>>(h2, W3g, b3c, h3);
-  k_tail<<<dim3(64, 114), 256, 0, stream>>>(h3, Wtail, btail, to, vsb, vA, vB);
-
-  k_msdeform<<<dim3(256, 8), 256, 0, stream>>>(vA, to, flow1, fcn2, featb);
-
-  k_opout<<<64, 256, 0, stream>>>(featb, o1b, op_b1, o2b, op_b2, x, (float*)d_out);
-}
+  KP P;
+  P.x     = (const float*)d_in[0];
+  P.flow1 = (const float*)d_in[1];
+  P.flow2 = (const float*)d_in[2];
+  P.aw_w1 = (const float*)d_in[5];  P.aw_b1 = (const float*)d_in[6];
+  P.aw_w2 = (const float*)d_in[7];  P.aw_b2 = (const float*)d_in[8];
+  P.aw_w3 = (const float*)d_in[9];  P.aw_b3 = (const float*)d_in[10];
+  P.aw_w4 = (const float*)d_in[11]; P.aw_b4 = (const float*)d_in[12];
+  P.so_w1 = (const float*)d_in[13]; P.so_b1 = (const float*)d_in[14];
+  P.so_w2 = (const float*)d_in[15]; P.so_b2 = (const float*)d_in[16];
+  P.so_w3 = (const float*)d_in[17]; P.so_b3 = (const float*)d_in[18];
+  P.so_w4 = (const float*)d_in[19]; P.so_b4 = (const float*)d_in[20];
+  P.po_w1 = (const float*)d_in[21]; P.po_b1 = (const float*)d_in[22];
+  P.po_w2 = (const float*)d_in[23]; P.po_b2 = (const float*)d_in[24];
+  P.po_w3 = (const float*)d_in[25]; P.po_b3 = (const float*)d_in[26];
+  P.po_w4 = (const float*)d_in[27]; P.po_b4 = (const float*)d_in[28];
+  P.vp_w  = (const float*)d_in[29]; P.vp_b  = (const float*)d_in[30];
+  P.op_w1 = (const float*)d_in[31]; P.op_b1 = (const float*)d_in[32];
+  P.op_w2 = (const float*)d_in[33]; P.op_b2 = (const float*)d_in[34];
+
+  P.fcn2  = (float*)alloc(2 * HWN * 4);
+  P.xb    = (unsigned short*)alloc(192 * HWN * 2);
+  P.vsb   = (unsigned short*)alloc(192 * HWN * 2);
+  P.extra = (unsigned short*)alloc(224 * HWN * 2);
+  P.h1    = (unsigned short*)alloc(192 * HWN * 2);
+  P.h2    = (unsigned short*)alloc(192 * HWN * 2);
+  P.h3    = (unsigned short*)alloc(192 * HWN * 2);
+  P.to    = (unsigned short*)alloc((size_t)3456 * HWN * 2);
+  P.featb = (unsigned short*)alloc(64 * HWN * 2);
+  P.v8    = (unsigned char*)alloc((size_t)VSZ_B * 2);
+  P.Wtail = (unsigned short*)alloc(3456 * 64 * 2);
+  P.btail = (float*)alloc(3456 * 4);
+  P.b1c   = (float*)alloc(192 * 4);
+  P.b2c   = (float*)alloc(192 * 4);
+  P.b3c   = (float*)alloc(192 * 4);
+  P.o1b   = (unsigned short*)alloc(64 * 64 * 2);
+  P.o2b   = (unsigned short*)alloc(64 * 64 * 2);
+  P.W1    = (unsigned short*)alloc(192 * 224 * 2);
+  P.W2g   = (unsigned short*)alloc(3 * 64 * 576 * 2);
+  P.W3g   = (unsigned short*)alloc(3 * 64 * 576 * 2);
+  P.vpb   = (unsigned short*)alloc(192 * 192 * 2);
+  P.out   = (float*)d_out;
+
+  int nbPerCU = 0;
+  hipError_t oe = hipOccupancyMaxActiveBlocksPerMultiprocessor(&nbPerCU, (const void*)k_all, 256, 0);
+  if (oe != hipSuccess || nbPerCU < 1) nbPerCU = 1;
+  int grid = nbPerCU * 256;
+  if (grid > 1024) grid = 1024;
+
+  void* args[] = {&P};
+  (void)hipLaunchCooperativeKernel((void*)k_all, dim3(grid), dim3(256), args, 0, stream);
+}
```

After: 694.1 us. +194.8%, slower.
